# Kernel optimization log

Measured on AMD Instinct MI355X. Metric: run time of the kernel, lower is better.

The kernel has to match this reference:

```python
import jax, jax.numpy as jnp
import numpy as np

N_NODES = 50000
N_EDGES = 800000
IN_DIM = 128
OUT_DIM = 128
NUM_RELS = 100
NUM_BASES = 4


def setup_inputs() -> dict:
    key = jax.random.key(0)
    ks = jax.random.split(key, 8)
    h = jax.random.normal(ks[0], (N_NODES, IN_DIM), dtype=jnp.float32)
    norm = jax.random.uniform(ks[1], (N_NODES, 1), dtype=jnp.float32)
    src = jax.random.randint(ks[2], (N_EDGES,), 0, N_NODES, dtype=jnp.int32)
    dst = jax.random.randint(ks[3], (N_EDGES,), 0, N_NODES, dtype=jnp.int32)
    rel_type = jax.random.randint(ks[4], (N_EDGES,), 0, NUM_RELS, dtype=jnp.int32)
    basis_weights = jax.random.normal(ks[5], (NUM_BASES, IN_DIM, OUT_DIM), dtype=jnp.float32) * (2.0 / np.sqrt(IN_DIM + OUT_DIM))
    coefficients = jax.random.normal(ks[6], (NUM_RELS, NUM_BASES), dtype=jnp.float32) * (1.0 / np.sqrt(NUM_RELS + NUM_BASES))
    loop_weight = jax.random.normal(ks[7], (IN_DIM, OUT_DIM), dtype=jnp.float32) * (2.0 / np.sqrt(IN_DIM + OUT_DIM))
    return {
        'h': h, 'norm': norm, 'src': src, 'dst': dst, 'rel_type': rel_type,
        'basis_weights': basis_weights, 'coefficients': coefficients,
        'loop_weight': loop_weight,
    }


def reference(h, norm, src, dst, rel_type, basis_weights, coefficients, loop_weight):
    # h: (N, in), norm: (N, 1), src/dst/rel_type: (E,)
    # basis_weights: (B, in, out), coefficients: (R, B), loop_weight: (in, out)
    n_nodes = h.shape[0]
    num_bases = basis_weights.shape[0]

    # self-loop message (dropout=0 -> identity)
    loop_message = h @ loop_weight  # (N, out)

    # W[r] = sum_b coeff[r, b] * basis[b]; per-edge msg_e = h[src_e] @ W[rel_e].
    # Reassociated: project nodes by each basis once, then mix per edge by
    # the relation coefficients -- identical math, avoids the (E, in, out)
    # gathered weight tensor of the original per-edge bmm.
    hb = jnp.einsum('ni,bio->bno', h, basis_weights)  # (B, N, out)
    c_e = coefficients[rel_type]  # (E, B)
    msg = c_e[:, 0, None] * hb[0][src]
    for b in range(1, num_bases):  # small fixed basis count
        msg = msg + c_e[:, b, None] * hb[b][src]  # (E, out)

    # scatter-sum aggregation to destination nodes, then norm scaling
    agg = jax.ops.segment_sum(msg, dst, num_segments=n_nodes)  # (N, out)
    node_repr = agg * norm  # _apply_func
    node_repr = node_repr + loop_message  # self-loop (bias=None)
    return jax.nn.relu(node_repr)  # activation
```

## Files before the change

### kernel.cpp

```cpp
#include <hip/hip_runtime.h>

typedef short bf16x8 __attribute__((ext_vector_type(8)));
typedef float floatx4 __attribute__((ext_vector_type(4)));
typedef float floatx2 __attribute__((ext_vector_type(2)));

typedef const __attribute__((address_space(1))) void* gas_ptr;
typedef __attribute__((address_space(3))) void* las_ptr;

#define EPB  4096
#define MAXB 6144

__device__ __forceinline__ unsigned short f2bf(float f) {
    unsigned int u = __float_as_uint(f);
    unsigned int r = u + 0x7fffu + ((u >> 16) & 1u);
    return (unsigned short)(r >> 16);
}

__device__ __forceinline__ void stage16(const void* g, void* lbase, int lane) {
#if __has_builtin(__builtin_amdgcn_global_load_lds)
    __builtin_amdgcn_global_load_lds((gas_ptr)g, (las_ptr)lbase, 16, 0, 0);
#else
    *(float4*)((char*)lbase + lane * 16) = *(const float4*)g;
#endif
}

__global__ __launch_bounds__(256) void prep_all(
    const float* __restrict__ h, unsigned short* __restrict__ hbf, int nconv,
    const int* __restrict__ dst, int* __restrict__ gh, int E, int nB, int nblkH,
    const float* __restrict__ basis, const float* __restrict__ loopw,
    unsigned short* __restrict__ WT2, int nb_conv)
{
    __shared__ int lh[256];
    const int b = blockIdx.x;
    const int t = threadIdx.x;
    if (b < nb_conv) {
        int idx = b * 256 + t;
        if (idx < nconv) {
            float2 v = *(const float2*)(h + (size_t)idx * 2);
            unsigned int pack = (unsigned int)f2bf(v.x) | ((unsigned int)f2bf(v.y) << 16);
            *(unsigned int*)(hbf + (size_t)idx * 2) = pack;
        }
    } else if (b < nb_conv + nblkH) {
        const int blk = b - nb_conv;
        if (t < nB) lh[t] = 0;
        __syncthreads();
        const int cbase = blk * EPB;
#pragma unroll
        for (int j = 0; j < EPB / 256; ++j) {
            int e = cbase + j * 256 + t;
            if (e < E) atomicAdd(&lh[dst[e] >> 8], 1);
        }
        __syncthreads();
        if (t < nB) gh[(size_t)t * nblkH + blk] = lh[t];
    } else {
        int c = b - nb_conv - nblkH;
        for (int k = t; k < 640; k += 256) {
            float v;
            if (k < 512) v = basis[(size_t)k * 128 + c];
            else         v = loopw[(size_t)(k - 512) * 128 + c];
            WT2[(size_t)c * 640 + k] = f2bf(v);
        }
    }
}

__global__ __launch_bounds__(256) void scan1(
    const int* __restrict__ in, int* __restrict__ bsum, int M)
{
    __shared__ int s[256];
    int i = blockIdx.x * 256 + threadIdx.x;
    int t = threadIdx.x;
    s[t] = (i < M) ? in[i] : 0;
    __syncthreads();
    for (int o = 128; o > 0; o >>= 1) {
        if (t < o) s[t] += s[t + o];
        __syncthreads();
    }
    if (t == 0) bsum[blockIdx.x] = s[0];
}

__global__ __launch_bounds__(256) void scan_final(
    const int* __restrict__ in, const int* __restrict__ bsum,
    int* __restrict__ out, int M)
{
    __shared__ int s[256];
    __shared__ int sb[256];
    int t = threadIdx.x;
    int i = blockIdx.x * 256 + t;
    sb[t] = (t < (int)blockIdx.x) ? bsum[t] : 0;
    int v = (i < M) ? in[i] : 0;
    s[t] = v;
    __syncthreads();
    for (int o = 128; o > 0; o >>= 1) {
        if (t < o) sb[t] += sb[t + o];
        __syncthreads();
    }
    for (int o = 1; o < 256; o <<= 1) {
        int x = (t >= o) ? s[t - o] : 0;
        __syncthreads();
        s[t] += x;
        __syncthreads();
    }
    if (i < M) out[i] = s[t] - v + sb[0];
}

__global__ __launch_bounds__(256) void scatter_bkt(
    const int* __restrict__ dst, const int* __restrict__ src,
    const int* __restrict__ rel, const int* __restrict__ sgh,
    unsigned int* __restrict__ tmp, int E, int nB, int nblkH)
{
    __shared__ int cur[256];
    const int blk = blockIdx.x;
    const int t = threadIdx.x;
    if (t < nB) cur[t] = sgh[(size_t)t * nblkH + blk];
    __syncthreads();
    const int cbase = blk * EPB;
#pragma unroll
    for (int j = 0; j < EPB / 256; ++j) {
        int e = cbase + j * 256 + t;
        if (e < E) {
            int d = dst[e];
            int slot = atomicAdd(&cur[d >> 8], 1);
            tmp[slot] = (unsigned int)src[e] | ((unsigned int)rel[e] << 16)
                      | ((unsigned int)(d & 255) << 23);
        }
    }
}

__global__ __launch_bounds__(256) void bucket_sort(
    const unsigned int* __restrict__ tmp, const int* __restrict__ sgh,
    unsigned int* __restrict__ sedge, int* __restrict__ rowptr,
    int E, int N, int nB, int nblkH)
{
    __shared__ unsigned int eb[MAXB];
    __shared__ int hh[256], ss[256], cur[256];
    const int b = blockIdx.x;
    const int t = threadIdx.x;
    const int brow = sgh[(size_t)b * nblkH];
    const int next = (b + 1 < nB) ? sgh[(size_t)(b + 1) * nblkH] : E;
    int n = next - brow;
    if (n > MAXB) n = MAXB;
    hh[t] = 0;
    __syncthreads();
    for (int i = t; i < n; i += 256) {
        unsigned int v = tmp[brow + i];
        eb[i] = v;
        atomicAdd(&hh[(v >> 23) & 255], 1);
    }
    __syncthreads();
    int v = hh[t];
    ss[t] = v;
    __syncthreads();
    for (int o = 1; o < 256; o <<= 1) {
        int x = (t >= o) ? ss[t - o] : 0;
        __syncthreads();
        ss[t] += x;
        __syncthreads();
    }
    const int excl = ss[t] - v;
    const int idx = b * 256 + t;
    if (idx <= N) rowptr[idx] = brow + excl;
    cur[t] = excl;
    __syncthreads();
    for (int i = t; i < n; i += 256) {
        unsigned int e = eb[i];
        int slot = atomicAdd(&cur[(e >> 23) & 255], 1);
        sedge[brow + slot] = ((e & 0xFFFFu) << 8) | (((e >> 16) & 0x7Fu) << 25);
    }
}

__global__ __launch_bounds__(256) void aggregate_pre(
    const unsigned short* __restrict__ hbf,
    const int* __restrict__ rowptr,
    const unsigned int* __restrict__ sedge,
    const float* __restrict__ coeff,
    const float* __restrict__ norm,
    unsigned short* __restrict__ A2, int N, int R)
{
    __shared__ float scoef[512];
    for (int i = threadIdx.x; i < R * 4; i += 256) scoef[i] = coeff[i];
    __syncthreads();

    const int wave = threadIdx.x >> 6;
    const int lane = threadIdx.x & 63;
    const int d = blockIdx.x * 4 + wave;
    if (d >= N) return;
    int i = rowptr[d];
    const int end = rowptr[d + 1];

    const char* hbase = (const char*)hbf + lane * 4;

    floatx2 a0 = {0.f, 0.f}, a1 = {0.f, 0.f}, a2 = {0.f, 0.f}, a3 = {0.f, 0.f};

#define EDGE_LOAD(v, u) \
    unsigned int u = *(const unsigned int*)(hbase + ((v) & 0x00FFFF00u));
#define EDGE_MATH(v, u) { \
    const float4 c = *(const float4*)((const char*)scoef + (((v) >> 25) << 4)); \
    floatx2 hp; \
    hp[0] = __uint_as_float((u) << 16); \
    hp[1] = __uint_as_float((u) & 0xFFFF0000u); \
    a0 = __builtin_elementwise_fma((floatx2){c.x, c.x}, hp, a0); \
    a1 = __builtin_elementwise_fma((floatx2){c.y, c.y}, hp, a1); \
    a2 = __builtin_elementwise_fma((floatx2){c.z, c.z}, hp, a2); \
    a3 = __builtin_elementwise_fma((floatx2){c.w, c.w}, hp, a3); }

    while (i < end && (i & 3)) {
        unsigned int v = sedge[i];
        EDGE_LOAD(v, u)
        EDGE_MATH(v, u)
        ++i;
    }
    for (; i + 8 <= end; i += 8) {
        uint4 e0 = *(const uint4*)(sedge + i);
        uint4 e1 = *(const uint4*)(sedge + i + 4);
        EDGE_LOAD(e0.x, u0) EDGE_LOAD(e0.y, u1) EDGE_LOAD(e0.z, u2) EDGE_LOAD(e0.w, u3)
        EDGE_LOAD(e1.x, u4) EDGE_LOAD(e1.y, u5) EDGE_LOAD(e1.z, u6) EDGE_LOAD(e1.w, u7)
        EDGE_MATH(e0.x, u0) EDGE_MATH(e0.y, u1) EDGE_MATH(e0.z, u2) EDGE_MATH(e0.w, u3)
        EDGE_MATH(e1.x, u4) EDGE_MATH(e1.y, u5) EDGE_MATH(e1.z, u6) EDGE_MATH(e1.w, u7)
    }
    for (; i + 4 <= end; i += 4) {
        uint4 e0 = *(const uint4*)(sedge + i);
        EDGE_LOAD(e0.x, u0) EDGE_LOAD(e0.y, u1) EDGE_LOAD(e0.z, u2) EDGE_LOAD(e0.w, u3)
        EDGE_MATH(e0.x, u0) EDGE_MATH(e0.y, u1) EDGE_MATH(e0.z, u2) EDGE_MATH(e0.w, u3)
    }
    for (; i < end; ++i) {
        unsigned int v = sedge[i];
        EDGE_LOAD(v, u)
        EDGE_MATH(v, u)
    }
#undef EDGE_LOAD
#undef EDGE_MATH

    const float nm = norm[d];
    unsigned short* row = A2 + (size_t)d * 512 + lane * 2;
    *(unsigned int*)(row)       = (unsigned int)f2bf(a0[0] * nm) | ((unsigned int)f2bf(a0[1] * nm) << 16);
    *(unsigned int*)(row + 128) = (unsigned int)f2bf(a1[0] * nm) | ((unsigned int)f2bf(a1[1] * nm) << 16);
    *(unsigned int*)(row + 256) = (unsigned int)f2bf(a2[0] * nm) | ((unsigned int)f2bf(a2[1] * nm) << 16);
    *(unsigned int*)(row + 384) = (unsigned int)f2bf(a3[0] * nm) | ((unsigned int)f2bf(a3[1] * nm) << 16);
}

__global__ __launch_bounds__(256) void final_gemm(
    const unsigned short* __restrict__ A2,
    const unsigned short* __restrict__ hbf,
    const unsigned short* __restrict__ WT2,
    float* __restrict__ out, int N)
{
    __shared__ char sA[16384];
    __shared__ char sB[16384];
    const int t = threadIdx.x;
    const int w = t >> 6;
    const int lane = t & 63;
    const int quad = lane >> 4;
    const int low  = lane & 15;
    const int wr = w >> 1, wc = w & 1;
    const int m0 = blockIdx.x * 128;

    floatx4 acc[4][4];
#pragma unroll
    for (int mt = 0; mt < 4; ++mt)
#pragma unroll
        for (int nt = 0; nt < 4; ++nt) acc[mt][nt] = (floatx4){0.f, 0.f, 0.f, 0.f};

    for (int it = 0; it < 10; ++it) {
        const int k0 = it * 64;
#pragma unroll
        for (int i = 0; i < 4; ++i) {
            const int slot = i * 256 + t;
            const int kc  = slot >> 7;
            const int idx = slot & 127;
            int grow = m0 + idx;
            if (grow >= N) grow = N - 1;
            const unsigned short* gA = (k0 < 512)
                ? A2  + (size_t)grow * 512 + k0 + kc * 8
                : hbf + (size_t)grow * 128 + (k0 - 512) + kc * 8;
            const unsigned short* gB = WT2 + (size_t)idx * 640 + k0 + kc * 8;
            stage16(gA, sA + (size_t)(i * 256 + w * 64) * 16, lane);
            stage16(gB, sB + (size_t)(i * 256 + w * 64) * 16, lane);
        }
        __syncthreads();

#pragma unroll
        for (int ks = 0; ks < 2; ++ks) {
            bf16x8 af[4], bfr[4];
#pragma unroll
            for (int mt = 0; mt < 4; ++mt)
                af[mt] = *(const bf16x8*)(sA + (size_t)(((ks * 4 + quad) << 7) + wr * 64 + mt * 16 + low) * 16);
#pragma unroll
            for (int nt = 0; nt < 4; ++nt)
                bfr[nt] = *(const bf16x8*)(sB + (size_t)(((ks * 4 + quad) << 7) + wc * 64 + nt * 16 + low) * 16);
#pragma unroll
            for (int mt = 0; mt < 4; ++mt)
#pragma unroll
                for (int nt = 0; nt < 4; ++nt)
                    acc[mt][nt] = __builtin_amdgcn_mfma_f32_16x16x32_bf16(af[mt], bfr[nt], acc[mt][nt], 0, 0, 0);
        }
        __syncthreads();
    }

#pragma unroll
    for (int mt = 0; mt < 4; ++mt) {
#pragma unroll
        for (int nt = 0; nt < 4; ++nt) {
            const int c = wc * 64 + nt * 16 + low;
#pragma unroll
            for (int r = 0; r < 4; ++r) {
                int rr = m0 + wr * 64 + mt * 16 + quad * 4 + r;
                if (rr < N) out[(size_t)rr * 128 + c] = fmaxf(acc[mt][nt][r], 0.f);
            }
        }
    }
}

extern "C" void kernel_launch(void* const* d_in, const int* in_sizes, int n_in,
                              void* d_out, int out_size, void* d_ws, size_t ws_size,
                              hipStream_t stream)
{
    const float* h     = (const float*)d_in[0];
    const float* norm  = (const float*)d_in[1];
    const int*   src   = (const int*)d_in[2];
    const int*   dst   = (const int*)d_in[3];
    const int*   rel   = (const int*)d_in[4];
    const float* basis = (const float*)d_in[5];
    const float* coeff = (const float*)d_in[6];
    const float* loopw = (const float*)d_in[7];
    float* out = (float*)d_out;

    const int N = in_sizes[1];
    const int E = in_sizes[2];
    const int R = in_sizes[6] / 4;

    const int nB    = (N + 255) >> 8;
    const int nblkH = (E + EPB - 1) / EPB;
    const int M     = nB * nblkH;
    const int NBs   = (M + 255) / 256;

    char* ws = (char*)d_ws;
    size_t off = 0;
    auto walloc = [&](size_t bytes) -> char* {
        char* p = ws + off;
        off = (off + bytes + 255) & ~(size_t)255;
        return p;
    };
    unsigned short* A2     = (unsigned short*)walloc((size_t)N * 512 * 2);
    unsigned short* hbf    = (unsigned short*)walloc((size_t)N * 128 * 2);
    unsigned short* WT2    = (unsigned short*)walloc(128 * 640 * 2);
    int*            rowptr = (int*)walloc((size_t)(N + 1) * 4);
    int*            bsum   = (int*)walloc((size_t)NBs * 4);
    int*            gh     = (int*)walloc((size_t)M * 4);
    int*            sgh    = (int*)walloc((size_t)M * 4);
    unsigned int*   tmp    = (unsigned int*)walloc((size_t)E * 4);
    unsigned int*   sedge  = (unsigned int*)walloc((size_t)E * 4);

    const int nconv = N * 64;
    const int nb_conv = (nconv + 255) / 256;

    prep_all<<<nb_conv + nblkH + 128, 256, 0, stream>>>(
        h, hbf, nconv, dst, gh, E, nB, nblkH, basis, loopw, WT2, nb_conv);
    scan1<<<NBs, 256, 0, stream>>>(gh, bsum, M);
    scan_final<<<NBs, 256, 0, stream>>>(gh, bsum, sgh, M);
    scatter_bkt<<<nblkH, 256, 0, stream>>>(dst, src, rel, sgh, tmp, E, nB, nblkH);
    bucket_sort<<<nB, 256, 0, stream>>>(tmp, sgh, sedge, rowptr, E, N, nB, nblkH);
    aggregate_pre<<<(N + 3) / 4, 256, 0, stream>>>(hbf, rowptr, sedge, coeff, norm, A2, N, R);
    final_gemm<<<(N + 127) / 128, 256, 0, stream>>>(A2, hbf, WT2, out, N);
}
```

Before: 205.1 us.

## Fold histogram scan into scatter and fuse aggregation with final GEMM

Drops the two separate scan kernels. Each scatter block now recomputes its own bin prefix from the per-block histogram, and block 0 publishes the bin starts used by the bucket sort. The edge aggregation and the MFMA GEMM are merged into one kernel: each 128-row block first aggregates its own 32 nodes per wave into A2, then runs the GEMM on those rows. This removes three launches and their gaps, but it cuts the aggregation grid from thousands of blocks to a few hundred, which risks poor latency hiding for the gather-bound phase.

```diff
diff --git a/kernel.cpp b/kernel.cpp
--- a/kernel.cpp
+++ b/kernel.cpp
@@ -42,7 +42,7 @@
         }
     } else if (b < nb_conv + nblkH) {
         const int blk = b - nb_conv;
-        if (t < nB) lh[t] = 0;
+        lh[t] = 0;
         __syncthreads();
         const int cbase = blk * EPB;
 #pragma unroll
@@ -63,60 +63,48 @@
     }
 }
 
-__global__ __launch_bounds__(256) void scan1(
-    const int* __restrict__ in, int* __restrict__ bsum, int M)
-{
-    __shared__ int s[256];
-    int i = blockIdx.x * 256 + threadIdx.x;
-    int t = threadIdx.x;
-    s[t] = (i < M) ? in[i] : 0;
-    __syncthreads();
-    for (int o = 128; o > 0; o >>= 1) {
-        if (t < o) s[t] += s[t + o];
-        __syncthreads();
-    }
-    if (t == 0) bsum[blockIdx.x] = s[0];
-}
-
-__global__ __launch_bounds__(256) void scan_final(
-    const int* __restrict__ in, const int* __restrict__ bsum,
-    int* __restrict__ out, int M)
-{
-    __shared__ int s[256];
-    __shared__ int sb[256];
-    int t = threadIdx.x;
-    int i = blockIdx.x * 256 + t;
-    sb[t] = (t < (int)blockIdx.x) ? bsum[t] : 0;
-    int v = (i < M) ? in[i] : 0;
-    s[t] = v;
-    __syncthreads();
-    for (int o = 128; o > 0; o >>= 1) {
-        if (t < o) sb[t] += sb[t + o];
-        __syncthreads();
-    }
-    for (int o = 1; o < 256; o <<= 1) {
-        int x = (t >= o) ? s[t - o] : 0;
-        __syncthreads();
-        s[t] += x;
-        __syncthreads();
-    }
-    if (i < M) out[i] = s[t] - v + sb[0];
-}
-
 __global__ __launch_bounds__(256) void scatter_bkt(
     const int* __restrict__ dst, const int* __restrict__ src,
-    const int* __restrict__ rel, const int* __restrict__ sgh,
-    unsigned int* __restrict__ tmp, int E, int nB, int nblkH)
-{
+    const int* __restrict__ rel, const int* __restrict__ gh,
+    int* __restrict__ binStart, unsigned int* __restrict__ tmp,
+    int E, int nB, int nblkH)
+{
+    __shared__ int ss[256];
     __shared__ int cur[256];
-    const int blk = blockIdx.x;
+    const int j = blockIdx.x;
     const int t = threadIdx.x;
-    if (t < nB) cur[t] = sgh[(size_t)t * nblkH + blk];
-    __syncthreads();
-    const int cbase = blk * EPB;
-#pragma unroll
-    for (int j = 0; j < EPB / 256; ++j) {
-        int e = cbase + j * 256 + t;
+
+    int pre = 0, tot = 0;
+    if (t < nB) {
+        const int* row = gh + (size_t)t * nblkH;
+#pragma unroll 8
+        for (int c = 0; c < nblkH; ++c) {
+            int v = row[c];
+            tot += v;
+            if (c < j) pre += v;
+        }
+    }
+    int v = (t < nB) ? tot : 0;
+    ss[t] = v;
+    __syncthreads();
+    for (int o = 1; o < 256; o <<= 1) {
+        int x = (t >= o) ? ss[t - o] : 0;
+        __syncthreads();
+        ss[t] += x;
+        __syncthreads();
+    }
+    const int gstart = ss[t] - v;
+    cur[t] = gstart + pre;
+    if (j == 0) {
+        if (t < nB) binStart[t] = gstart;
+        if (t == 0) binStart[nB] = E;
+    }
+    __syncthreads();
+
+    const int cbase = j * EPB;
+#pragma unroll
+    for (int jj = 0; jj < EPB / 256; ++jj) {
+        int e = cbase + jj * 256 + t;
         if (e < E) {
             int d = dst[e];
             int slot = atomicAdd(&cur[d >> 8], 1);
@@ -127,16 +115,16 @@
 }
 
 __global__ __launch_bounds__(256) void bucket_sort(
-    const unsigned int* __restrict__ tmp, const int* __restrict__ sgh,
+    const unsigned int* __restrict__ tmp, const int* __restrict__ binStart,
     unsigned int* __restrict__ sedge, int* __restrict__ rowptr,
-    int E, int N, int nB, int nblkH)
+    int E, int N, int nB)
 {
     __shared__ unsigned int eb[MAXB];
     __shared__ int hh[256], ss[256], cur[256];
     const int b = blockIdx.x;
     const int t = threadIdx.x;
-    const int brow = sgh[(size_t)b * nblkH];
-    const int next = (b + 1 < nB) ? sgh[(size_t)(b + 1) * nblkH] : E;
+    const int brow = binStart[b];
+    const int next = binStart[b + 1];
     int n = next - brow;
     if (n > MAXB) n = MAXB;
     hh[t] = 0;
@@ -168,28 +156,36 @@
     }
 }
 
-__global__ __launch_bounds__(256) void aggregate_pre(
+__global__ __launch_bounds__(256) void agg_gemm(
     const unsigned short* __restrict__ hbf,
     const int* __restrict__ rowptr,
     const unsigned int* __restrict__ sedge,
     const float* __restrict__ coeff,
     const float* __restrict__ norm,
-    unsigned short* __restrict__ A2, int N, int R)
-{
-    __shared__ float scoef[512];
-    for (int i = threadIdx.x; i < R * 4; i += 256) scoef[i] = coeff[i];
-    __syncthreads();
-
-    const int wave = threadIdx.x >> 6;
-    const int lane = threadIdx.x & 63;
-    const int d = blockIdx.x * 4 + wave;
-    if (d >= N) return;
-    int i = rowptr[d];
-    const int end = rowptr[d + 1];
-
-    const char* hbase = (const char*)hbf + lane * 4;
-
-    floatx2 a0 = {0.f, 0.f}, a1 = {0.f, 0.f}, a2 = {0.f, 0.f}, a3 = {0.f, 0.f};
+    unsigned short* __restrict__ A2,
+    const unsigned short* __restrict__ WT2,
+    float* __restrict__ out, int N, int R)
+{
+    __shared__ alignas(16) unsigned char smem[32768];
+    const int t = threadIdx.x;
+    const int m0 = blockIdx.x * 128;
+
+    {
+        float* scoef = (float*)smem;
+        for (int i = t; i < R * 4; i += 256) scoef[i] = coeff[i];
+        __syncthreads();
+
+        const int wave = t >> 6;
+        const int lane = t & 63;
+        const char* hbase = (const char*)hbf + lane * 4;
+
+        for (int k = 0; k < 32; ++k) {
+            const int d = m0 + wave * 32 + k;
+            if (d >= N) break;
+            int i = rowptr[d];
+            const int end = rowptr[d + 1];
+
+            floatx2 a0 = {0.f, 0.f}, a1 = {0.f, 0.f}, a2 = {0.f, 0.f}, a3 = {0.f, 0.f};
 
 #define EDGE_LOAD(v, u) \
     unsigned int u = *(const unsigned int*)(hbase + ((v) & 0x00FFFF00u));
@@ -203,108 +199,103 @@
     a2 = __builtin_elementwise_fma((floatx2){c.z, c.z}, hp, a2); \
     a3 = __builtin_elementwise_fma((floatx2){c.w, c.w}, hp, a3); }
 
-    while (i < end && (i & 3)) {
-        unsigned int v = sedge[i];
-        EDGE_LOAD(v, u)
-        EDGE_MATH(v, u)
-        ++i;
-    }
-    for (; i + 8 <= end; i += 8) {
-        uint4 e0 = *(const uint4*)(sedge + i);
-        uint4 e1 = *(const uint4*)(sedge + i + 4);
-        EDGE_LOAD(e0.x, u0) EDGE_LOAD(e0.y, u1) EDGE_LOAD(e0.z, u2) EDGE_LOAD(e0.w, u3)
-        EDGE_LOAD(e1.x, u4) EDGE_LOAD(e1.y, u5) EDGE_LOAD(e1.z, u6) EDGE_LOAD(e1.w, u7)
-        EDGE_MATH(e0.x, u0) EDGE_MATH(e0.y, u1) EDGE_MATH(e0.z, u2) EDGE_MATH(e0.w, u3)
-        EDGE_MATH(e1.x, u4) EDGE_MATH(e1.y, u5) EDGE_MATH(e1.z, u6) EDGE_MATH(e1.w, u7)
-    }
-    for (; i + 4 <= end; i += 4) {
-        uint4 e0 = *(const uint4*)(sedge + i);
-        EDGE_LOAD(e0.x, u0) EDGE_LOAD(e0.y, u1) EDGE_LOAD(e0.z, u2) EDGE_LOAD(e0.w, u3)
-        EDGE_MATH(e0.x, u0) EDGE_MATH(e0.y, u1) EDGE_MATH(e0.z, u2) EDGE_MATH(e0.w, u3)
-    }
-    for (; i < end; ++i) {
-        unsigned int v = sedge[i];
-        EDGE_LOAD(v, u)
-        EDGE_MATH(v, u)
-    }
+            while (i < end && (i & 3)) {
+                unsigned int v = sedge[i];
+                EDGE_LOAD(v, u)
+                EDGE_MATH(v, u)
+                ++i;
+            }
+            for (; i + 8 <= end; i += 8) {
+                uint4 e0 = *(const uint4*)(sedge + i);
+                uint4 e1 = *(const uint4*)(sedge + i + 4);
+                EDGE_LOAD(e0.x, u0) EDGE_LOAD(e0.y, u1) EDGE_LOAD(e0.z, u2) EDGE_LOAD(e0.w, u3)
+                EDGE_LOAD(e1.x, u4) EDGE_LOAD(e1.y, u5) EDGE_LOAD(e1.z, u6) EDGE_LOAD(e1.w, u7)
+                EDGE_MATH(e0.x, u0) EDGE_MATH(e0.y, u1) EDGE_MATH(e0.z, u2) EDGE_MATH(e0.w, u3)
+                EDGE_MATH(e1.x, u4) EDGE_MATH(e1.y, u5) EDGE_MATH(e1.z, u6) EDGE_MATH(e1.w, u7)
+            }
+            for (; i + 4 <= end; i += 4) {
+                uint4 e0 = *(const uint4*)(sedge + i);
+                EDGE_LOAD(e0.x, u0) EDGE_LOAD(e0.y, u1) EDGE_LOAD(e0.z, u2) EDGE_LOAD(e0.w, u3)
+                EDGE_MATH(e0.x, u0) EDGE_MATH(e0.y, u1) EDGE_MATH(e0.z, u2) EDGE_MATH(e0.w, u3)
+            }
+            for (; i < end; ++i) {
+                unsigned int v = sedge[i];
+                EDGE_LOAD(v, u)
+                EDGE_MATH(v, u)
+            }
 #undef EDGE_LOAD
 #undef EDGE_MATH
 
-    const float nm = norm[d];
-    unsigned short* row = A2 + (size_t)d * 512 + lane * 2;
-    *(unsigned int*)(row)       = (unsigned int)f2bf(a0[0] * nm) | ((unsigned int)f2bf(a0[1] * nm) << 16);
-    *(unsigned int*)(row + 128) = (unsigned int)f2bf(a1[0] * nm) | ((unsigned int)f2bf(a1[1] * nm) << 16);
-    *(unsigned int*)(row + 256) = (unsigned int)f2bf(a2[0] * nm) | ((unsigned int)f2bf(a2[1] * nm) << 16);
-    *(unsigned int*)(row + 384) = (unsigned int)f2bf(a3[0] * nm) | ((unsigned int)f2bf(a3[1] * nm) << 16);
-}
-
-__global__ __launch_bounds__(256) void final_gemm(
-    const unsigned short* __restrict__ A2,
-    const unsigned short* __restrict__ hbf,
-    const unsigned short* __restrict__ WT2,
-    float* __restrict__ out, int N)
-{
-    __shared__ char sA[16384];
-    __shared__ char sB[16384];
-    const int t = threadIdx.x;
-    const int w = t >> 6;
-    const int lane = t & 63;
-    const int quad = lane >> 4;
-    const int low  = lane & 15;
-    const int wr = w >> 1, wc = w & 1;
-    const int m0 = blockIdx.x * 128;
-
-    floatx4 acc[4][4];
-#pragma unroll
-    for (int mt = 0; mt < 4; ++mt)
-#pragma unroll
-        for (int nt = 0; nt < 4; ++nt) acc[mt][nt] = (floatx4){0.f, 0.f, 0.f, 0.f};
-
-    for (int it = 0; it < 10; ++it) {
-        const int k0 = it * 64;
-#pragma unroll
-        for (int i = 0; i < 4; ++i) {
-            const int slot = i * 256 + t;
-            const int kc  = slot >> 7;
-            const int idx = slot & 127;
-            int grow = m0 + idx;
-            if (grow >= N) grow = N - 1;
-            const unsigned short* gA = (k0 < 512)
-                ? A2  + (size_t)grow * 512 + k0 + kc * 8
-                : hbf + (size_t)grow * 128 + (k0 - 512) + kc * 8;
-            const unsigned short* gB = WT2 + (size_t)idx * 640 + k0 + kc * 8;
-            stage16(gA, sA + (size_t)(i * 256 + w * 64) * 16, lane);
-            stage16(gB, sB + (size_t)(i * 256 + w * 64) * 16, lane);
-        }
-        __syncthreads();
-
-#pragma unroll
-        for (int ks = 0; ks < 2; ++ks) {
-            bf16x8 af[4], bfr[4];
-#pragma unroll
-            for (int mt = 0; mt < 4; ++mt)
-                af[mt] = *(const bf16x8*)(sA + (size_t)(((ks * 4 + quad) << 7) + wr * 64 + mt * 16 + low) * 16);
-#pragma unroll
-            for (int nt = 0; nt < 4; ++nt)
-                bfr[nt] = *(const bf16x8*)(sB + (size_t)(((ks * 4 + quad) << 7) + wc * 64 + nt * 16 + low) * 16);
-#pragma unroll
-            for (int mt = 0; mt < 4; ++mt)
+            const float nm = norm[d];
+            unsigned short* row = A2 + (size_t)d * 512 + lane * 2;
+            *(unsigned int*)(row)       = (unsigned int)f2bf(a0[0] * nm) | ((unsigned int)f2bf(a0[1] * nm) << 16);
+            *(unsigned int*)(row + 128) = (unsigned int)f2bf(a1[0] * nm) | ((unsigned int)f2bf(a1[1] * nm) << 16);
+            *(unsigned int*)(row + 256) = (unsigned int)f2bf(a2[0] * nm) | ((unsigned int)f2bf(a2[1] * nm) << 16);
+            *(unsigned int*)(row + 384) = (unsigned int)f2bf(a3[0] * nm) | ((unsigned int)f2bf(a3[1] * nm) << 16);
+        }
+    }
+    __syncthreads();
+
+    {
+        char* sA = (char*)smem;
+        char* sB = (char*)smem + 16384;
+        const int w = t >> 6;
+        const int lane = t & 63;
+        const int quad = lane >> 4;
+        const int low  = lane & 15;
+        const int wr = w >> 1, wc = w & 1;
+
+        floatx4 acc[4][4];
+#pragma unroll
+        for (int mt = 0; mt < 4; ++mt)
+#pragma unroll
+            for (int nt = 0; nt < 4; ++nt) acc[mt][nt] = (floatx4){0.f, 0.f, 0.f, 0.f};
+
+        for (int it = 0; it < 10; ++it) {
+            const int k0 = it * 64;
+#pragma unroll
+            for (int i = 0; i < 4; ++i) {
+                const int slot = i * 256 + t;
+                const int kc  = slot >> 7;
+                const int idx = slot & 127;
+                int grow = m0 + idx;
+                if (grow >= N) grow = N - 1;
+                const unsigned short* gA = (k0 < 512)
+                    ? A2  + (size_t)grow * 512 + k0 + kc * 8
+                    : hbf + (size_t)grow * 128 + (k0 - 512) + kc * 8;
+                const unsigned short* gB = WT2 + (size_t)idx * 640 + k0 + kc * 8;
+                stage16(gA, sA + (size_t)(i * 256 + w * 64) * 16, lane);
+                stage16(gB, sB + (size_t)(i * 256 + w * 64) * 16, lane);
+            }
+            __syncthreads();
+#pragma unroll
+            for (int ks = 0; ks < 2; ++ks) {
+                bf16x8 af[4], bfr[4];
+#pragma unroll
+                for (int mt = 0; mt < 4; ++mt)
+                    af[mt] = *(const bf16x8*)(sA + (size_t)(((ks * 4 + quad) << 7) + wr * 64 + mt * 16 + low) * 16);
 #pragma unroll
                 for (int nt = 0; nt < 4; ++nt)
-                    acc[mt][nt] = __builtin_amdgcn_mfma_f32_16x16x32_bf16(af[mt], bfr[nt], acc[mt][nt], 0, 0, 0);
-        }
-        __syncthreads();
-    }
-
-#pragma unroll
-    for (int mt = 0; mt < 4; ++mt) {
-#pragma unroll
-        for (int nt = 0; nt < 4; ++nt) {
-            const int c = wc * 64 + nt * 16 + low;
-#pragma unroll
-            for (int r = 0; r < 4; ++r) {
-                int rr = m0 + wr * 64 + mt * 16 + quad * 4 + r;
-                if (rr < N) out[(size_t)rr * 128 + c] = fmaxf(acc[mt][nt][r], 0.f);
+                    bfr[nt] = *(const bf16x8*)(sB + (size_t)(((ks * 4 + quad) << 7) + wc * 64 + nt * 16 + low) * 16);
+#pragma unroll
+                for (int mt = 0; mt < 4; ++mt)
+#pragma unroll
+                    for (int nt = 0; nt < 4; ++nt)
+                        acc[mt][nt] = __builtin_amdgcn_mfma_f32_16x16x32_bf16(af[mt], bfr[nt], acc[mt][nt], 0, 0, 0);
+            }
+            __syncthreads();
+        }
+
+#pragma unroll
+        for (int mt = 0; mt < 4; ++mt) {
+#pragma unroll
+            for (int nt = 0; nt < 4; ++nt) {
+                const int c = wc * 64 + nt * 16 + low;
+#pragma unroll
+                for (int r = 0; r < 4; ++r) {
+                    int rr = m0 + wr * 64 + mt * 16 + quad * 4 + r;
+                    if (rr < N) out[(size_t)rr * 128 + c] = fmaxf(acc[mt][nt][r], 0.f);
+                }
             }
         }
     }
@@ -328,10 +319,10 @@
     const int E = in_sizes[2];
     const int R = in_sizes[6] / 4;
 
-    const int nB    = (N + 255) >> 8;
-    const int nblkH = (E + EPB - 1) / EPB;
-    const int M     = nB * nblkH;
-    const int NBs   = (M + 255) / 256;
+    const int nB      = (N + 255) >> 8;
+    const int nblkH   = (E + EPB - 1) / EPB;
+    const int M       = nB * nblkH;
+    const int nb_conv = (N * 64 + 255) / 256;
 
     char* ws = (char*)d_ws;
     size_t off = 0;
@@ -340,25 +331,20 @@
         off = (off + bytes + 255) & ~(size_t)255;
         return p;
     };
-    unsigned short* A2     = (unsigned short*)walloc((size_t)N * 512 * 2);
-    unsigned short* hbf    = (unsigned short*)walloc((size_t)N * 128 * 2);
-    unsigned short* WT2    = (unsigned short*)walloc(128 * 640 * 2);
-    int*            rowptr = (int*)walloc((size_t)(N + 1) * 4);
-    int*            bsum   = (int*)walloc((size_t)NBs * 4);
-    int*            gh     = (int*)walloc((size_t)M * 4);
-    int*            sgh    = (int*)walloc((size_t)M * 4);
-    unsigned int*   tmp    = (unsigned int*)walloc((size_t)E * 4);
-    unsigned int*   sedge  = (unsigned int*)walloc((size_t)E * 4);
-
-    const int nconv = N * 64;
-    const int nb_conv = (nconv + 255) / 256;
+    unsigned short* A2       = (unsigned short*)walloc((size_t)N * 512 * 2);
+    unsigned short* hbf      = (unsigned short*)walloc((size_t)N * 128 * 2);
+    unsigned short* WT2      = (unsigned short*)walloc(128 * 640 * 2);
+    int*            gh       = (int*)walloc((size_t)M * 4);
+    int*            binStart = (int*)walloc((size_t)(nB + 1) * 4);
+    unsigned int*   tmp      = (unsigned int*)walloc((size_t)E * 4);
+    unsigned int*   sedge    = (unsigned int*)walloc((size_t)E * 4);
+    int*            rowptr   = (int*)walloc((size_t)(N + 1) * 4);
 
     prep_all<<<nb_conv + nblkH + 128, 256, 0, stream>>>(
-        h, hbf, nconv, dst, gh, E, nB, nblkH, basis, loopw, WT2, nb_conv);
-    scan1<<<NBs, 256, 0, stream>>>(gh, bsum, M);
-    scan_final<<<NBs, 256, 0, stream>>>(gh, bsum, sgh, M);
-    scatter_bkt<<<nblkH, 256, 0, stream>>>(dst, src, rel, sgh, tmp, E, nB, nblkH);
-    bucket_sort<<<nB, 256, 0, stream>>>(tmp, sgh, sedge, rowptr, E, N, nB, nblkH);
-    aggregate_pre<<<(N + 3) / 4, 256, 0, stream>>>(hbf, rowptr, sedge, coeff, norm, A2, N, R);
-    final_gemm<<<(N + 127) / 128, 256, 0, stream>>>(A2, hbf, WT2, out, N);
-}
+        h, hbf, nb_conv * 256 < N * 64 ? N * 64 : N * 64, dst, gh, E, nB, nblkH,
+        basis, loopw, WT2, nb_conv);
+    scatter_bkt<<<nblkH, 256, 0, stream>>>(dst, src, rel, gh, binStart, tmp, E, nB, nblkH);
+    bucket_sort<<<nB, 256, 0, stream>>>(tmp, binStart, sedge, rowptr, E, N, nB);
+    agg_gemm<<<(N + 127) / 128, 256, 0, stream>>>(
+        hbf, rowptr, sedge, coeff, norm, A2, WT2, out, N, R);
+}
```

After: 280.7 us. 36.8% more time.
